# Performance work log

Measured on AMD Instinct MI355X. Metric: run time of the kernel, lower is better.

## Reference

```python
import jax, jax.numpy as jnp
import numpy as np

R = 16
EPS = 1e-6
OFFSETS = (1, 2, 4, 8, 16, 32)
_IDX_I, _IDX_J = np.triu_indices(R, k=1)  # plu_dim = 120


def _plucker(u, v):
    # u, v: (B, L, r) -> (B, L, plu_dim), normalized with eps-clamped norm
    p = u[..., _IDX_I] * v[..., _IDX_J] - u[..., _IDX_J] * v[..., _IDX_I]
    norm = jnp.maximum(jnp.linalg.norm(p, axis=-1, keepdims=True), EPS)
    return p / norm


def setup_inputs() -> dict:
    key = jax.random.key(0)
    ks = jax.random.split(key, 6)
    B, L, D, d_geom = 4, 4096, 1024, 256
    plu_dim = R * (R - 1) // 2
    s = lambda fan_in: 1.0 / np.sqrt(fan_in)
    return {
        "h": jax.random.normal(ks[0], (B, L, D), jnp.float32),
        "red_w": jax.random.normal(ks[1], (D, R), jnp.float32) * s(D),
        "red_b": jnp.zeros((R,), jnp.float32),
        "g1_w": jax.random.normal(ks[2], (plu_dim, d_geom), jnp.float32) * s(plu_dim),
        "g1_b": jnp.zeros((d_geom,), jnp.float32),
        "g2_w": jax.random.normal(ks[3], (d_geom, D), jnp.float32) * s(d_geom),
        "g2_b": jnp.zeros((D,), jnp.float32),
        "gate_w": jax.random.normal(ks[4], (2 * D, D), jnp.float32) * s(2 * D),
        "gate_b": jnp.zeros((D,), jnp.float32),
    }


def reference(h, red_w, red_b, g1_w, g1_b, g2_w, g2_b, gate_w, gate_b):
    B, L, D = h.shape
    z = h @ red_w + red_b  # (B, L, r)
    geom_sum = jnp.zeros((B, L, D), h.dtype)
    count = jnp.zeros((B, L, 1), h.dtype)
    pos = jnp.arange(L)
    for delta in OFFSETS:
        if delta >= L:
            continue
        # causal shift: z_past[t] = z[t - delta], zero-padded
        z_past = jnp.pad(z[:, : L - delta], ((0, 0), (delta, 0), (0, 0)))
        p = _plucker(z_past, z)  # (B, L, plu_dim)
        g_delta = jax.nn.gelu(p @ g1_w + g1_b, approximate=False) @ g2_w + g2_b
        mask = (pos >= delta).astype(h.dtype)[None, :, None]  # (1, L, 1)
        geom_sum = geom_sum + g_delta * mask
        count = count + jnp.broadcast_to(mask, (B, L, 1))
    g = geom_sum / jnp.maximum(count, 1.0)
    alpha = jax.nn.sigmoid(jnp.concatenate([h, g], axis=-1) @ gate_w + gate_b)
    return alpha * h + (1.0 - alpha) * g
```

## Files before the change

### kernel.cpp

```cpp
#include <hip/hip_runtime.h>
#include <hip/hip_bf16.h>
#include <math.h>

typedef unsigned short u16;
typedef unsigned int u32;
typedef __attribute__((ext_vector_type(8))) short short8;
typedef __attribute__((ext_vector_type(4))) float f32x4;

#define L_SEQ 4096
#define N_TOK 16384
#define D_MODEL 1024
#define R_DIM 16
#define PLU 120
#define G_DIM 256
#define K_CAT 1536
#define K_GATE 2048

typedef __attribute__((address_space(1))) const void* as1cvp;
typedef __attribute__((address_space(3))) void* as3vp;
#define GLD16(g, l) \
  __builtin_amdgcn_global_load_lds((as1cvp)(g), (as3vp)(l), 16, 0, 0)

#define CFENCE asm volatile("" ::: "memory")
#define BARB                        \
  {                                 \
    CFENCE;                         \
    __builtin_amdgcn_s_barrier();   \
    CFENCE;                         \
  }
#define VM0 asm volatile("s_waitcnt vmcnt(0)" ::: "memory")

__device__ __forceinline__ u16 f2bf(float f) {
  u32 x = __float_as_uint(f);
  u32 lsb = (x >> 16) & 1u;
  x += 0x7fffu + lsb;
  return (u16)(x >> 16);
}
__device__ __forceinline__ float bf2f(u16 u) {
  return __uint_as_float(((u32)u) << 16);
}
__device__ __forceinline__ u32 pack2(float a, float b) {
  return (u32)f2bf(a) | ((u32)f2bf(b) << 16);
}

__device__ __forceinline__ float gelu_erf(float x) {
  const float y = x * 0.70710678118654752f;
  const float a = fabsf(y);
  const float t = __builtin_amdgcn_rcpf(fmaf(0.3275911f, a, 1.0f));
  float poly = fmaf(1.061405429f, t, -1.453152027f);
  poly = fmaf(poly, t, 1.421413741f);
  poly = fmaf(poly, t, -0.284496736f);
  poly = fmaf(poly, t, 0.254829592f);
  poly *= t;
  const float e = __builtin_amdgcn_exp2f(-1.4426950408889634f * a * a);
  float er = fmaf(-poly, e, 1.0f);
  er = copysignf(er, y);
  const float hx = 0.5f * x;
  return fmaf(hx, er, hx);
}

constexpr int PLU_I[PLU] = {
    0, 0, 0, 0, 0, 0, 0, 0, 0, 0, 0, 0, 0, 0, 0,
    1, 1, 1, 1, 1, 1, 1, 1, 1, 1, 1, 1, 1, 1,
    2, 2, 2, 2, 2, 2, 2, 2, 2, 2, 2, 2, 2,
    3, 3, 3, 3, 3, 3, 3, 3, 3, 3, 3, 3,
    4, 4, 4, 4, 4, 4, 4, 4, 4, 4, 4,
    5, 5, 5, 5, 5, 5, 5, 5, 5, 5,
    6, 6, 6, 6, 6, 6, 6, 6, 6,
    7, 7, 7, 7, 7, 7, 7, 7,
    8, 8, 8, 8, 8, 8, 8,
    9, 9, 9, 9, 9, 9,
    10, 10, 10, 10, 10,
    11, 11, 11, 11,
    12, 12, 12,
    13, 13,
    14};
constexpr int PLU_J[PLU] = {
    1, 2, 3, 4, 5, 6, 7, 8, 9, 10, 11, 12, 13, 14, 15,
    2, 3, 4, 5, 6, 7, 8, 9, 10, 11, 12, 13, 14, 15,
    3, 4, 5, 6, 7, 8, 9, 10, 11, 12, 13, 14, 15,
    4, 5, 6, 7, 8, 9, 10, 11, 12, 13, 14, 15,
    5, 6, 7, 8, 9, 10, 11, 12, 13, 14, 15,
    6, 7, 8, 9, 10, 11, 12, 13, 14, 15,
    7, 8, 9, 10, 11, 12, 13, 14, 15,
    8, 9, 10, 11, 12, 13, 14, 15,
    9, 10, 11, 12, 13, 14, 15,
    10, 11, 12, 13, 14, 15,
    11, 12, 13, 14, 15,
    12, 13, 14, 15,
    13, 14, 15,
    14, 15,
    15};

__global__ __launch_bounds__(256) void k_cvtT(const float* __restrict__ src,
                                              u16* __restrict__ dst, int K,
                                              int Kp, int N) {
  __shared__ float t[32][33];
  const int k0 = blockIdx.y * 32, n0 = blockIdx.x * 32;
  const int r = threadIdx.x >> 3, c4 = (threadIdx.x & 7) * 4;
  float4 v = {0.f, 0.f, 0.f, 0.f};
  if (k0 + r < K) v = *(const float4*)(src + (size_t)(k0 + r) * N + n0 + c4);
  t[r][c4] = v.x;
  t[r][c4 + 1] = v.y;
  t[r][c4 + 2] = v.z;
  t[r][c4 + 3] = v.w;
  __syncthreads();
  uint2 o;
  o.x = pack2(t[c4][r], t[c4 + 1][r]);
  o.y = pack2(t[c4 + 2][r], t[c4 + 3][r]);
  *(uint2*)(dst + (size_t)(n0 + r) * Kp + k0 + c4) = o;
}

__global__ __launch_bounds__(256) void k_reduce(const float* __restrict__ h,
                                                const float* __restrict__ red_w,
                                                const float* __restrict__ red_b,
                                                float* __restrict__ z,
                                                u16* __restrict__ hb) {
  __shared__ alignas(16) u16 hs[16 * D_MODEL];
  const int tid = threadIdx.x;
  const int t0 = blockIdx.x * 16;

  const float4* src = (const float4*)(h + (size_t)t0 * D_MODEL);
  u32* dst = (u32*)hs;
#pragma unroll
  for (int it = 0; it < (16 * D_MODEL / 4) / 256; ++it) {
    const int idx = tid + it * 256;
    const float4 v = src[idx];
    dst[idx * 2 + 0] = pack2(v.x, v.y);
    dst[idx * 2 + 1] = pack2(v.z, v.w);
  }
  __syncthreads();

  {
    const uint4* s4 = (const uint4*)hs;
    uint4* d4 = (uint4*)(hb + (size_t)t0 * D_MODEL);
#pragma unroll
    for (int it = 0; it < (16 * D_MODEL / 8) / 256; ++it)
      d4[tid + it * 256] = s4[tid + it * 256];
  }

  const int m = tid >> 4, c = tid & 15;
  const u16* hrow = hs + m * D_MODEL;
  float acc = 0.f;
#pragma unroll 8
  for (int i = 0; i < D_MODEL; i += 2) {
    u32 hv = *(const u32*)(hrow + i);
    float h0 = __uint_as_float(hv << 16);
    float h1 = __uint_as_float(hv & 0xffff0000u);
    acc = fmaf(h0, red_w[i * R_DIM + c], acc);
    acc = fmaf(h1, red_w[(i + 1) * R_DIM + c], acc);
  }
  z[(size_t)(t0 + m) * R_DIM + c] = acc + red_b[c];
}

#define PLUG(G)                                                               \
  _Pragma("unroll") for (int cc = 0; cc < 2; ++cc) {                          \
    u32 ow[4];                                                                \
    _Pragma("unroll") for (int eo = 0; eo < 4; ++eo) {                        \
      float pp[2];                                                            \
      _Pragma("unroll") for (int e2 = 0; e2 < 2; ++e2) {                      \
        const int k = ((G)*2 + cc) * 8 + eo * 2 + e2;                         \
        float p = 0.f;                                                        \
        if (k < PLU) {                                                        \
          p = zp[PLU_I[k]] * zcr[PLU_J[k]] - zp[PLU_J[k]] * zcr[PLU_I[k]];    \
          s = fmaf(p, p, s);                                                  \
        }                                                                     \
        pp[e2] = p;                                                           \
      }                                                                       \
      ow[eo] = pack2(pp[0], pp[1]);                                           \
    }                                                                         \
    *(uint4*)&pb[((((G)*2 + cc) ^ rsw) * 8)] = *(uint4*)ow;                   \
  }

__global__ __launch_bounds__(512) void k_plu(const float* __restrict__ z,
                                             const u16* __restrict__ W1t,
                                             const float* __restrict__ g1b,
                                             u16* __restrict__ A, int t0g) {
  __shared__ alignas(16) float zx[96][17];
  __shared__ alignas(16) u16 W1s[128][128];
  __shared__ alignas(16) u16 Pb[64][128];
  __shared__ float prt[64][8];
  __shared__ float rno[64];
  __shared__ float b1s[128];

  const int tid = threadIdx.x, lane = tid & 63, w = tid >> 6;
  const int wm = w >> 2, wn = w & 3;
  const int n0 = blockIdx.x * 128;
  const int tl = blockIdx.y * 64;
  const int tg = t0g + tl;
  const int l0 = tg & (L_SEQ - 1);
  const int mr = lane & 15;
  const int qlane = lane >> 4;

  if (tid < 128) b1s[tid] = g1b[n0 + tid];
  for (int r = tid; r < 96 * 16; r += 512) {
    const int rr = r >> 4, c = r & 15;
    int t = tg - 32 + rr;
    if (t < 0) t = 0;
    zx[rr][c] = z[(size_t)t * R_DIM + c];
  }
  {
    const uint4* src = (const uint4*)(W1t + (size_t)n0 * 128);
    for (int i = tid; i < 128 * 16; i += 512) {
      const int r = i >> 4, c = i & 15;
      *(uint4*)&W1s[r][(c ^ (r & 15)) * 8] = src[i];
    }
  }
  __syncthreads();

  float zcr[R_DIM];
  {
    const float* zc = zx[32 + lane];
#pragma unroll
    for (int c = 0; c < R_DIM; ++c) zcr[c] = zc[c];
  }

  f32x4 acc[2][2];

#pragma unroll 1
  for (int dd = 0; dd < 6; ++dd) {
    const int delta = 1 << dd;
    if (dd) __syncthreads();
    {
      const int row = lane;
      const int rsw = lane & 15;
      const float* zpr = zx[32 + row - delta];
      float zp[R_DIM];
#pragma unroll
      for (int c = 0; c < R_DIM; ++c) zp[c] = zpr[c];
      float s = 0.f;
      u16* pb = &Pb[row][0];
      switch (w) {
        case 0: PLUG(0); break;
        case 1: PLUG(1); break;
        case 2: PLUG(2); break;
        case 3: PLUG(3); break;
        case 4: PLUG(4); break;
        case 5: PLUG(5); break;
        case 6: PLUG(6); break;
        default: PLUG(7); break;
      }
      prt[row][w] = s;
    }
    __syncthreads();
    if (tid < 64) {
      const float s = prt[tid][0] + prt[tid][1] + prt[tid][2] + prt[tid][3] +
                      prt[tid][4] + prt[tid][5] + prt[tid][6] + prt[tid][7];
      rno[tid] = 1.0f / fmaxf(sqrtf(s), 1e-6f);
    }
    __syncthreads();
#pragma unroll
    for (int a = 0; a < 2; ++a)
#pragma unroll
      for (int b = 0; b < 2; ++b) acc[a][b] = (f32x4)(0.f);
#pragma unroll
    for (int k0 = 0; k0 < 128; k0 += 32) {
      const int ci = (k0 >> 3) + qlane;
      short8 af[2], bfr[2];
#pragma unroll
      for (int mi = 0; mi < 2; ++mi) {
        const int r = wm * 32 + mi * 16 + mr;
        af[mi] = *(const short8*)&Pb[r][(ci ^ (r & 15)) * 8];
      }
#pragma unroll
      for (int ni = 0; ni < 2; ++ni) {
        const int r = wn * 32 + ni * 16 + mr;
        bfr[ni] = *(const short8*)&W1s[r][(ci ^ (r & 15)) * 8];
      }
#pragma unroll
      for (int mi = 0; mi < 2; ++mi)
#pragma unroll
        for (int ni = 0; ni < 2; ++ni)
          acc[mi][ni] = __builtin_amdgcn_mfma_f32_16x16x32_bf16(
              af[mi], bfr[ni], acc[mi][ni], 0, 0, 0);
    }
#pragma unroll
    for (int mi = 0; mi < 2; ++mi) {
#pragma unroll
      for (int r = 0; r < 4; ++r) {
        const int rowl = wm * 32 + mi * 16 + qlane * 4 + r;
        const bool ok = (l0 + rowl) >= delta;
        const float rn = rno[rowl];
#pragma unroll
        for (int ni = 0; ni < 2; ++ni) {
          const int colL = wn * 32 + ni * 16 + mr;
          const float x = acc[mi][ni][r] * rn + b1s[colL];
          const float ge = gelu_erf(x);
          A[(size_t)(tl + rowl) * K_CAT + dd * G_DIM + n0 + colL] =
              ok ? f2bf(ge) : (u16)0;
        }
      }
    }
  }
}


#define COMP                                                                  \
  {                                                                           \
    _Pragma("unroll") for (int kk = 0; kk < 2; ++kk) {                        \
      short8 af[4], bfr[4];                                                   \
      _Pragma("unroll") for (int mi = 0; mi < 4; ++mi) {                      \
        const int r = wm * 64 + mi * 16 + mr;                                 \
        af[mi] = *(const short8*)&lds[r * 64 +                                \
                                      (((qlane + kk * 4) ^ (r & 7)) << 3)];   \
      }                                                                       \
      _Pragma("unroll") for (int ni = 0; ni < 4; ++ni) {                      \
        const int r = wn * 64 + ni * 16 + mr;                                 \
        bfr[ni] = *(const short8*)&lds[8192 + r * 64 +                        \
                                       (((qlane + kk * 4) ^ (r & 7)) << 3)];  \
      }                                                                       \
      _Pragma("unroll") for (int mi = 0; mi < 4; ++mi)                        \
          _Pragma("unroll") for (int ni = 0; ni < 4; ++ni) acc[mi][ni] =      \
          __builtin_amdgcn_mfma_f32_16x16x32_bf16(af[mi], bfr[ni],            \
                                                  acc[mi][ni], 0, 0, 0);      \
    }                                                                         \
  }

__global__ __launch_bounds__(256, 4) void k_gemm2(const u16* __restrict__ A,
                                                  const u16* __restrict__ W2t,
                                                  const float* __restrict__ g2b,
                                                  u16* __restrict__ g,
                                                  int t0g) {
  __shared__ alignas(16) u16 lds[16384];
  const int tid = threadIdx.x, lane = tid & 63, w = tid >> 6;
  const int wm = w >> 1, wn = w & 1;

  const int cpx = (int)gridDim.x >> 3;
  const int wi = ((int)blockIdx.x & 7) * cpx + ((int)blockIdx.x >> 3);
  const int n0 = (wi & 7) << 7;
  const int ml = (wi >> 3) << 7;

  const int lr3 = lane >> 3, lc = lane & 7;
  const int koff = (lc ^ lr3) << 3;
  const int rb = w * 32 + lr3;
  const u16* a0 = A + (size_t)(ml + rb) * K_CAT + koff;
  const u16* b0 = W2t + (size_t)(n0 + rb) * G_DIM + koff;

#define STA(T)                                                                \
  _Pragma("unroll") for (int q = 0; q < 4; ++q)                               \
      GLD16(a0 + (size_t)(q * 8) * K_CAT + (T)*64,                            \
            lds + (w * 32 + q * 8) * 64);
#define STB(T)                                                                \
  _Pragma("unroll") for (int q = 0; q < 4; ++q)                               \
      GLD16(b0 + (size_t)(q * 8) * G_DIM + (((T)*64) & (G_DIM - 1)),          \
            lds + 8192 + (w * 32 + q * 8) * 64);

  const int qlane = lane >> 4, mr = lane & 15;

  f32x4 acc[4][4];
#pragma unroll
  for (int a = 0; a < 4; ++a)
#pragma unroll
    for (int b = 0; b < 4; ++b) acc[a][b] = (f32x4)(0.f);

  const int NT = K_CAT / 64;
  STA(0);
  STB(0);
  VM0;
  BARB;
#pragma unroll 1
  for (int t = 0; t < NT; ++t) {
    COMP;
    if (t + 1 < NT) {
      BARB;
      STA(t + 1);
      STB(t + 1);
      VM0;
      BARB;
    }
  }

  const int colb = n0 + wn * 64 + mr;
#pragma unroll
  for (int mi = 0; mi < 4; ++mi) {
#pragma unroll
    for (int r = 0; r < 4; ++r) {
      const int rowl = ml + wm * 64 + mi * 16 + qlane * 4 + r;
      const int l = (t0g + rowl) & (L_SEQ - 1);
      const float cnt = (float)((l >= 1) + (l >= 2) + (l >= 4) + (l >= 8) +
                                (l >= 16) + (l >= 32));
      const float inv = 1.0f / fmaxf(cnt, 1.0f);
#pragma unroll
      for (int ni = 0; ni < 4; ++ni) {
        const int col = colb + ni * 16;
        const float v = (acc[mi][ni][r] + cnt * g2b[col]) * inv;
        g[(size_t)rowl * D_MODEL + col] = f2bf(v);
      }
    }
  }
#undef STA
#undef STB
}

__global__ __launch_bounds__(256, 4) void k_gate(const u16* __restrict__ hb,
                                                 const u16* __restrict__ g,
                                                 const u16* __restrict__ WtG,
                                                 const float* __restrict__ gb,
                                                 float* __restrict__ out,
                                                 int t0g) {
  __shared__ alignas(16) u16 lds[16384];
  const int tid = threadIdx.x, lane = tid & 63, w = tid >> 6;
  const int wm = w >> 1, wn = w & 1;

  const int cpx = (int)gridDim.x >> 3;
  const int wi = ((int)blockIdx.x & 7) * cpx + ((int)blockIdx.x >> 3);
  const int n0 = (wi & 7) << 7;
  const int ml = (wi >> 3) << 7;

  const int lr3 = lane >> 3, lc = lane & 7;
  const int koff = (lc ^ lr3) << 3;
  const int rb = w * 32 + lr3;
  const u16* ph = hb + (size_t)(t0g + ml + rb) * D_MODEL + koff;
  const u16* pg = g + (size_t)(ml + rb) * D_MODEL + koff;
  const u16* pb = WtG + (size_t)(n0 + rb) * K_GATE + koff;

#define STA(T)                                                                \
  {                                                                           \
    const u16* s_ = ((T) < 16 ? ph : pg) + (size_t)((T)&15) * 64;             \
    _Pragma("unroll") for (int q = 0; q < 4; ++q)                             \
        GLD16(s_ + (size_t)(q * 8) * D_MODEL,                                 \
              lds + (w * 32 + q * 8) * 64);                                   \
  }
#define STB(T)                                                                \
  _Pragma("unroll") for (int q = 0; q < 4; ++q)                               \
      GLD16(pb + (size_t)(q * 8) * K_GATE + (T)*64,                           \
            lds + 8192 + (w * 32 + q * 8) * 64);

  const int qlane = lane >> 4, mr = lane & 15;

  f32x4 acc[4][4];
#pragma unroll
  for (int a = 0; a < 4; ++a)
#pragma unroll
    for (int b = 0; b < 4; ++b) acc[a][b] = (f32x4)(0.f);

  const int NT = K_GATE / 64;
  STA(0);
  STB(0);
  VM0;
  BARB;
#pragma unroll 1
  for (int t = 0; t < NT; ++t) {
    COMP;
    if (t + 1 < NT) {
      BARB;
      STA(t + 1);
      STB(t + 1);
      VM0;
      BARB;
    }
  }

  const int colb = n0 + wn * 64 + mr;
#pragma unroll
  for (int mi = 0; mi < 4; ++mi) {
#pragma unroll
    for (int r = 0; r < 4; ++r) {
      const int rowl = ml + wm * 64 + mi * 16 + qlane * 4 + r;
      const size_t rowg = (size_t)(t0g + rowl) * D_MODEL;
#pragma unroll
      for (int ni = 0; ni < 4; ++ni) {
        const int col = colb + ni * 16;
        const float x = acc[mi][ni][r] + gb[col];
        const float al = 1.0f / (1.0f + expf(-x));
        const float hv = bf2f(hb[rowg + col]);
        const float gv = bf2f(g[(size_t)rowl * D_MODEL + col]);
        out[rowg + col] = fmaf(al, hv - gv, gv);
      }
    }
  }
#undef STA
#undef STB
}

extern "C" void kernel_launch(void* const* d_in, const int* in_sizes, int n_in,
                              void* d_out, int out_size, void* d_ws,
                              size_t ws_size, hipStream_t stream) {
  const float* h = (const float*)d_in[0];
  const float* red_w = (const float*)d_in[1];
  const float* red_b = (const float*)d_in[2];
  const float* g1w = (const float*)d_in[3];
  const float* g1b = (const float*)d_in[4];
  const float* g2w = (const float*)d_in[5];
  const float* g2b = (const float*)d_in[6];
  const float* gate_w = (const float*)d_in[7];
  const float* gate_b = (const float*)d_in[8];
  float* out = (float*)d_out;

  const size_t sz_z = ((size_t)N_TOK * R_DIM * 4 + 255) & ~(size_t)255;
  const size_t sz_hb = (size_t)N_TOK * D_MODEL * 2;
  const size_t sz_WtG = (size_t)D_MODEL * K_GATE * 2;
  const size_t sz_W2t = (size_t)D_MODEL * G_DIM * 2;
  const size_t sz_W1t = (size_t)G_DIM * 128 * 2;
  const size_t fixed = sz_z + sz_hb + sz_WtG + sz_W2t + sz_W1t + 4096;

  int nc = 1;
  for (; nc <= 8; nc *= 2) {
    const size_t ct = N_TOK / nc;
    if (fixed + ct * (size_t)K_CAT * 2 + ct * (size_t)D_MODEL * 2 <= ws_size)
      break;
  }
  if (nc > 8) nc = 8;
  const int ct = N_TOK / nc;

  char* p = (char*)d_ws;
  float* z = (float*)p;
  p += sz_z;
  u16* hb = (u16*)p;
  p += sz_hb;
  u16* WtG = (u16*)p;
  p += sz_WtG;
  u16* W2t = (u16*)p;
  p += sz_W2t;
  u16* W1t = (u16*)p;
  p += sz_W1t;
  u16* Abuf = (u16*)p;
  p += (size_t)ct * K_CAT * 2;
  u16* gbuf = (u16*)p;

  k_reduce<<<dim3(N_TOK / 16), 256, 0, stream>>>(h, red_w, red_b, z, hb);
  k_cvtT<<<dim3(G_DIM / 32, 128 / 32), 256, 0, stream>>>(g1w, W1t, PLU, 128,
                                                         G_DIM);
  k_cvtT<<<dim3(D_MODEL / 32, G_DIM / 32), 256, 0, stream>>>(g2w, W2t, G_DIM,
                                                             G_DIM, D_MODEL);
  k_cvtT<<<dim3(D_MODEL / 32, K_GATE / 32), 256, 0, stream>>>(
      gate_w, WtG, K_GATE, K_GATE, D_MODEL);

  for (int c = 0; c < nc; ++c) {
    const int t0g = c * ct;
    k_plu<<<dim3(2, ct / 64), 512, 0, stream>>>(z, W1t, g1b, Abuf, t0g);
    k_gemm2<<<dim3((ct / 128) * 8), 256, 0, stream>>>(Abuf, W2t, g2b, gbuf,
                                                      t0g);
    k_gate<<<dim3((ct / 128) * 8), 256, 0, stream>>>(hb, gbuf, WtG, gate_b,
                                                     out, t0g);
  }
}
```

Measured before the change: 339.3 us.

## Sum GELU outputs across offsets before second projection and fuse it into k_plu

Because the second geometric projection is linear, the masked GELU activations for all six offsets are now summed in fp32 registers before a single K=256 GEMM with W2. The bias is added as count times g2b. That GEMM is fused into k_plu, which removes the k_gemm2 kernel, its K=1536 reduction and the round trip of the large concatenated A buffer through global memory. In exchange, each block reads W1t and W2t fragments straight from global/L2 without LDS staging, keeps a large accumulator array in registers, and uses only one block per 64 tokens, which may cost occupancy.

```diff
diff --git a/kernel.cpp b/kernel.cpp
--- a/kernel.cpp
+++ b/kernel.cpp
@@ -13,7 +13,6 @@
 #define R_DIM 16
 #define PLU 120
 #define G_DIM 256
-#define K_CAT 1536
 #define K_GATE 2048
 
 typedef __attribute__((address_space(1))) const void* as1cvp;
@@ -174,38 +173,32 @@
 
 __global__ __launch_bounds__(512) void k_plu(const float* __restrict__ z,
                                              const u16* __restrict__ W1t,
+                                             const u16* __restrict__ W2t,
                                              const float* __restrict__ g1b,
-                                             u16* __restrict__ A, int t0g) {
+                                             const float* __restrict__ g2b,
+                                             u16* __restrict__ g, int t0g) {
   __shared__ alignas(16) float zx[96][17];
-  __shared__ alignas(16) u16 W1s[128][128];
   __shared__ alignas(16) u16 Pb[64][128];
+  __shared__ alignas(16) u16 Ad[64][256];
   __shared__ float prt[64][8];
   __shared__ float rno[64];
-  __shared__ float b1s[128];
+  __shared__ float b1s[G_DIM];
 
   const int tid = threadIdx.x, lane = tid & 63, w = tid >> 6;
   const int wm = w >> 2, wn = w & 3;
-  const int n0 = blockIdx.x * 128;
-  const int tl = blockIdx.y * 64;
+  const int tl = blockIdx.x * 64;
   const int tg = t0g + tl;
   const int l0 = tg & (L_SEQ - 1);
   const int mr = lane & 15;
   const int qlane = lane >> 4;
 
-  if (tid < 128) b1s[tid] = g1b[n0 + tid];
+  if (tid < G_DIM) b1s[tid] = g1b[tid];
   for (int r = tid; r < 96 * 16; r += 512) {
     const int rr = r >> 4, c = r & 15;
     int t = tg - 32 + rr;
     if (t < 0) t = 0;
     zx[rr][c] = z[(size_t)t * R_DIM + c];
   }
-  {
-    const uint4* src = (const uint4*)(W1t + (size_t)n0 * 128);
-    for (int i = tid; i < 128 * 16; i += 512) {
-      const int r = i >> 4, c = i & 15;
-      *(uint4*)&W1s[r][(c ^ (r & 15)) * 8] = src[i];
-    }
-  }
   __syncthreads();
 
   float zcr[R_DIM];
@@ -215,7 +208,11 @@
     for (int c = 0; c < R_DIM; ++c) zcr[c] = zc[c];
   }
 
-  f32x4 acc[2][2];
+  f32x4 as_acc[2][4];
+#pragma unroll
+  for (int a = 0; a < 2; ++a)
+#pragma unroll
+    for (int b = 0; b < 4; ++b) as_acc[a][b] = (f32x4)(0.f);
 
 #pragma unroll 1
   for (int dd = 0; dd < 6; ++dd) {
@@ -249,30 +246,32 @@
       rno[tid] = 1.0f / fmaxf(sqrtf(s), 1e-6f);
     }
     __syncthreads();
+
+    f32x4 acc1[2][4];
 #pragma unroll
     for (int a = 0; a < 2; ++a)
 #pragma unroll
-      for (int b = 0; b < 2; ++b) acc[a][b] = (f32x4)(0.f);
+      for (int b = 0; b < 4; ++b) acc1[a][b] = (f32x4)(0.f);
 #pragma unroll
     for (int k0 = 0; k0 < 128; k0 += 32) {
       const int ci = (k0 >> 3) + qlane;
-      short8 af[2], bfr[2];
+      short8 af[2], bfr[4];
 #pragma unroll
       for (int mi = 0; mi < 2; ++mi) {
         const int r = wm * 32 + mi * 16 + mr;
         af[mi] = *(const short8*)&Pb[r][(ci ^ (r & 15)) * 8];
       }
 #pragma unroll
-      for (int ni = 0; ni < 2; ++ni) {
-        const int r = wn * 32 + ni * 16 + mr;
-        bfr[ni] = *(const short8*)&W1s[r][(ci ^ (r & 15)) * 8];
+      for (int ni = 0; ni < 4; ++ni) {
+        const int r = wn * 64 + ni * 16 + mr;
+        bfr[ni] = *(const short8*)(W1t + (size_t)r * 128 + k0 + qlane * 8);
       }
 #pragma unroll
       for (int mi = 0; mi < 2; ++mi)
 #pragma unroll
-        for (int ni = 0; ni < 2; ++ni)
-          acc[mi][ni] = __builtin_amdgcn_mfma_f32_16x16x32_bf16(
-              af[mi], bfr[ni], acc[mi][ni], 0, 0, 0);
+        for (int ni = 0; ni < 4; ++ni)
+          acc1[mi][ni] = __builtin_amdgcn_mfma_f32_16x16x32_bf16(
+              af[mi], bfr[ni], acc1[mi][ni], 0, 0, 0);
     }
 #pragma unroll
     for (int mi = 0; mi < 2; ++mi) {
@@ -282,18 +281,78 @@
         const bool ok = (l0 + rowl) >= delta;
         const float rn = rno[rowl];
 #pragma unroll
-        for (int ni = 0; ni < 2; ++ni) {
-          const int colL = wn * 32 + ni * 16 + mr;
-          const float x = acc[mi][ni][r] * rn + b1s[colL];
+        for (int ni = 0; ni < 4; ++ni) {
+          const int colL = wn * 64 + ni * 16 + mr;
+          const float x = acc1[mi][ni][r] * rn + b1s[colL];
           const float ge = gelu_erf(x);
-          A[(size_t)(tl + rowl) * K_CAT + dd * G_DIM + n0 + colL] =
-              ok ? f2bf(ge) : (u16)0;
+          as_acc[mi][ni][r] += ok ? ge : 0.f;
         }
       }
     }
   }
-}
-
+
+#pragma unroll
+  for (int mi = 0; mi < 2; ++mi) {
+#pragma unroll
+    for (int r = 0; r < 4; ++r) {
+      const int rowl = wm * 32 + mi * 16 + qlane * 4 + r;
+#pragma unroll
+      for (int ni = 0; ni < 4; ++ni) {
+        const int colL = wn * 64 + ni * 16 + mr;
+        const int ch = colL >> 3;
+        const int swz = (ch & 24) | ((ch & 7) ^ (rowl & 7));
+        Ad[rowl][swz * 8 + (colL & 7)] = f2bf(as_acc[mi][ni][r]);
+      }
+    }
+  }
+  __syncthreads();
+
+  f32x4 acc2[4][8];
+#pragma unroll
+  for (int a = 0; a < 4; ++a)
+#pragma unroll
+    for (int b = 0; b < 8; ++b) acc2[a][b] = (f32x4)(0.f);
+#pragma unroll
+  for (int k0 = 0; k0 < 256; k0 += 32) {
+    const int ci = (k0 >> 3) + qlane;
+    const int swz = (ci & 24);
+    short8 af2[4], bf2[8];
+#pragma unroll
+    for (int mi = 0; mi < 4; ++mi) {
+      const int r = mi * 16 + mr;
+      af2[mi] = *(const short8*)&Ad[r][(swz | ((ci & 7) ^ (r & 7))) * 8];
+    }
+#pragma unroll
+    for (int fc = 0; fc < 8; ++fc) {
+      const int r = w * 128 + fc * 16 + mr;
+      bf2[fc] = *(const short8*)(W2t + (size_t)r * G_DIM + k0 + qlane * 8);
+    }
+#pragma unroll
+    for (int mi = 0; mi < 4; ++mi)
+#pragma unroll
+      for (int fc = 0; fc < 8; ++fc)
+        acc2[mi][fc] = __builtin_amdgcn_mfma_f32_16x16x32_bf16(
+            af2[mi], bf2[fc], acc2[mi][fc], 0, 0, 0);
+  }
+
+#pragma unroll
+  for (int mi = 0; mi < 4; ++mi) {
+#pragma unroll
+    for (int r = 0; r < 4; ++r) {
+      const int rowl = mi * 16 + qlane * 4 + r;
+      const int l = (tg + rowl) & (L_SEQ - 1);
+      const float cnt = (float)((l >= 1) + (l >= 2) + (l >= 4) + (l >= 8) +
+                                (l >= 16) + (l >= 32));
+      const float inv = 1.0f / fmaxf(cnt, 1.0f);
+#pragma unroll
+      for (int fc = 0; fc < 8; ++fc) {
+        const int col = w * 128 + fc * 16 + mr;
+        const float v = (acc2[mi][fc][r] + cnt * g2b[col]) * inv;
+        g[(size_t)(tl + rowl) * D_MODEL + col] = f2bf(v);
+      }
+    }
+  }
+}
 
 #define COMP                                                                  \
   {                                                                           \
@@ -316,82 +375,6 @@
     }                                                                         \
   }
 
-__global__ __launch_bounds__(256, 4) void k_gemm2(const u16* __restrict__ A,
-                                                  const u16* __restrict__ W2t,
-                                                  const float* __restrict__ g2b,
-                                                  u16* __restrict__ g,
-                                                  int t0g) {
-  __shared__ alignas(16) u16 lds[16384];
-  const int tid = threadIdx.x, lane = tid & 63, w = tid >> 6;
-  const int wm = w >> 1, wn = w & 1;
-
-  const int cpx = (int)gridDim.x >> 3;
-  const int wi = ((int)blockIdx.x & 7) * cpx + ((int)blockIdx.x >> 3);
-  const int n0 = (wi & 7) << 7;
-  const int ml = (wi >> 3) << 7;
-
-  const int lr3 = lane >> 3, lc = lane & 7;
-  const int koff = (lc ^ lr3) << 3;
-  const int rb = w * 32 + lr3;
-  const u16* a0 = A + (size_t)(ml + rb) * K_CAT + koff;
-  const u16* b0 = W2t + (size_t)(n0 + rb) * G_DIM + koff;
-
-#define STA(T)                                                                \
-  _Pragma("unroll") for (int q = 0; q < 4; ++q)                               \
-      GLD16(a0 + (size_t)(q * 8) * K_CAT + (T)*64,                            \
-            lds + (w * 32 + q * 8) * 64);
-#define STB(T)                                                                \
-  _Pragma("unroll") for (int q = 0; q < 4; ++q)                               \
-      GLD16(b0 + (size_t)(q * 8) * G_DIM + (((T)*64) & (G_DIM - 1)),          \
-            lds + 8192 + (w * 32 + q * 8) * 64);
-
-  const int qlane = lane >> 4, mr = lane & 15;
-
-  f32x4 acc[4][4];
-#pragma unroll
-  for (int a = 0; a < 4; ++a)
-#pragma unroll
-    for (int b = 0; b < 4; ++b) acc[a][b] = (f32x4)(0.f);
-
-  const int NT = K_CAT / 64;
-  STA(0);
-  STB(0);
-  VM0;
-  BARB;
-#pragma unroll 1
-  for (int t = 0; t < NT; ++t) {
-    COMP;
-    if (t + 1 < NT) {
-      BARB;
-      STA(t + 1);
-      STB(t + 1);
-      VM0;
-      BARB;
-    }
-  }
-
-  const int colb = n0 + wn * 64 + mr;
-#pragma unroll
-  for (int mi = 0; mi < 4; ++mi) {
-#pragma unroll
-    for (int r = 0; r < 4; ++r) {
-      const int rowl = ml + wm * 64 + mi * 16 + qlane * 4 + r;
-      const int l = (t0g + rowl) & (L_SEQ - 1);
-      const float cnt = (float)((l >= 1) + (l >= 2) + (l >= 4) + (l >= 8) +
-                                (l >= 16) + (l >= 32));
-      const float inv = 1.0f / fmaxf(cnt, 1.0f);
-#pragma unroll
-      for (int ni = 0; ni < 4; ++ni) {
-        const int col = colb + ni * 16;
-        const float v = (acc[mi][ni][r] + cnt * g2b[col]) * inv;
-        g[(size_t)rowl * D_MODEL + col] = f2bf(v);
-      }
-    }
-  }
-#undef STA
-#undef STB
-}
-
 __global__ __launch_bounds__(256, 4) void k_gate(const u16* __restrict__ hb,
                                                  const u16* __restrict__ g,
                                                  const u16* __restrict__ WtG,
@@ -497,8 +480,7 @@
   int nc = 1;
   for (; nc <= 8; nc *= 2) {
     const size_t ct = N_TOK / nc;
-    if (fixed + ct * (size_t)K_CAT * 2 + ct * (size_t)D_MODEL * 2 <= ws_size)
-      break;
+    if (fixed + ct * (size_t)D_MODEL * 2 <= ws_size) break;
   }
   if (nc > 8) nc = 8;
   const int ct = N_TOK / nc;
@@ -514,8 +496,6 @@
   p += sz_W2t;
   u16* W1t = (u16*)p;
   p += sz_W1t;
-  u16* Abuf = (u16*)p;
-  p += (size_t)ct * K_CAT * 2;
   u16* gbuf = (u16*)p;
 
   k_reduce<<<dim3(N_TOK / 16), 256, 0, stream>>>(h, red_w, red_b, z, hb);
@@ -528,9 +508,8 @@
 
   for (int c = 0; c < nc; ++c) {
     const int t0g = c * ct;
-    k_plu<<<dim3(2, ct / 64), 512, 0, stream>>>(z, W1t, g1b, Abuf, t0g);
-    k_gemm2<<<dim3((ct / 128) * 8), 256, 0, stream>>>(Abuf, W2t, g2b, gbuf,
-                                                      t0g);
+    k_plu<<<dim3(ct / 64), 512, 0, stream>>>(z, W1t, W2t, g1b, g2b, gbuf,
+                                             t0g);
     k_gate<<<dim3((ct / 128) * 8), 256, 0, stream>>>(hb, gbuf, WtG, gate_b,
                                                      out, t0g);
   }
```

After: 315.1 us. 7.1% less time.
